# Optimization experiments

Measured on AMD Instinct MI355X. Metric: run time of the kernel, lower is better.

Reference implementation:

```python
import jax, jax.numpy as jnp
import numpy as np

B, L, Q = 2, 512, 512
E, W, D, H_NLM = 1024, 1024, 8, 32
NH = 16
HD = E // NH
SA, SO = 512, 1024
V = 8192
T = 6  # max_thought_step
SYN_H = 2048


def setup_inputs() -> dict:
    key = jax.random.key(0)
    ks = jax.random.split(key, 24)
    n = lambda k, shp, s=0.02: jax.random.normal(k, shp, dtype=jnp.float32) * s
    return {
        "x": jax.random.randint(ks[0], (B, L), 0, V),
        "num_output_q": Q,
        "emb": n(ks[1], (V, E)),
        "w_kv": n(ks[2], (E, E)),
        "w_q_sync": n(ks[3], (SA, E)),
        "wq": n(ks[4], (E, E)),
        "wk": n(ks[5], (E, E)),
        "wv": n(ks[6], (E, E)),
        "wo": n(ks[7], (E, E)),
        "ws1": n(ks[8], (E + W, SYN_H)),
        "bs1": jnp.zeros((SYN_H,), jnp.float32),
        "ws2": n(ks[9], (SYN_H, W)),
        "bs2": jnp.zeros((W,), jnp.float32),
        "nlm_w1": n(ks[10], (W, D, H_NLM), 0.1),
        "nlm_b1": jnp.zeros((W, H_NLM), jnp.float32),
        "nlm_w2": n(ks[11], (W, H_NLM), 0.1),
        "nlm_b2": jnp.zeros((W,), jnp.float32),
        "out_w": n(ks[12], (SO, V)),
        "out_b": jnp.zeros((V,), jnp.float32),
        "z_init": jax.random.normal(ks[13], (W,), dtype=jnp.float32),
        "pah_init": jax.random.normal(ks[14], (W, D), dtype=jnp.float32),
        "decay_a": jnp.zeros((SA,), jnp.float32),
        "decay_o": jnp.zeros((SO,), jnp.float32),
        "idx_la": jax.random.randint(ks[15], (SA,), 0, W),
        "idx_ra": jax.random.randint(ks[16], (SA,), 0, W),
        "idx_lo": jax.random.randint(ks[17], (SO,), 0, W),
        "idx_ro": jax.random.randint(ks[18], (SO,), 0, W),
    }


def _rope(xh, pos):
    # xh: [B, NH, S, HD]; rotate-half RoPE
    half = HD // 2
    inv = 1.0 / (10000.0 ** (jnp.arange(half, dtype=jnp.float32) / half))
    ang = pos.astype(jnp.float32)[:, None] * inv[None, :]  # [S, half]
    cos, sin = jnp.cos(ang), jnp.sin(ang)
    x1, x2 = xh[..., :half], xh[..., half:]
    return jnp.concatenate([x1 * cos - x2 * sin, x2 * cos + x1 * sin], axis=-1)


def _attention(q_in, kv, wq, wk, wv, wo):
    # causal cross-attention with RoPE on q and k
    Bq, Sq, _ = q_in.shape
    Sk = kv.shape[1]
    heads = lambda t: t.reshape(t.shape[0], t.shape[1], NH, HD).transpose(0, 2, 1, 3)
    qh = _rope(heads(q_in @ wq), jnp.arange(Sq))
    kh = _rope(heads(kv @ wk), jnp.arange(Sk))
    vh = heads(kv @ wv)
    scores = jnp.einsum('bhqd,bhkd->bhqk', qh, kh) / jnp.sqrt(jnp.float32(HD))
    i = jnp.arange(Sq)[:, None]
    j = jnp.arange(Sk)[None, :]
    scores = jnp.where(j <= i + (Sk - Sq), scores, jnp.float32(-1e30))
    out = jnp.einsum('bhqk,bhkd->bhqd', jax.nn.softmax(scores, axis=-1), vh)
    return out.transpose(0, 2, 1, 3).reshape(Bq, Sq, E) @ wo


def _compute_sync(hist, idx_l, idx_r, decay):
    # hist: list of [B,Q,W]; exponentially-decayed gather-multiply-reduce over time
    seq = jnp.stack(hist, axis=1)  # [B, Tn, Q, W]
    Tn = seq.shape[1]
    t_back = jnp.arange(Tn - 1, -1, -1, dtype=jnp.float32).reshape(1, Tn, 1, 1)
    ed = jnp.exp(-t_back * decay.reshape(1, 1, 1, -1))  # [1,Tn,1,S]
    sm = seq[..., idx_l] * ed * seq[..., idx_r]  # [B,Tn,Q,S]
    return sm.sum(axis=1) / jnp.sqrt(ed.sum(axis=1))  # [B,Q,S]


def reference(x, num_output_q, emb, w_kv, w_q_sync, wq, wk, wv, wo, ws1, bs1, ws2, bs2,
              nlm_w1, nlm_b1, nlm_w2, nlm_b2, out_w, out_b, z_init, pah_init,
              decay_a, decay_o, idx_la, idx_ra, idx_lo, idx_ro):
    emb_input = emb[x]                      # [B,L,E]
    kv = emb_input @ w_kv                   # [B,L,E]
    pah = jnp.broadcast_to(pah_init, (B, Q, W, D))
    z = jnp.broadcast_to(z_init, (B, Q, W))
    hist = [z]
    sync_a = _compute_sync(hist, idx_la, idx_ra, decay_a)
    outs = []
    for _ in range(T):
        q = sync_a @ w_q_sync               # [B,Q,E]
        attn_out = _attention(q, kv, wq, wk, wv, wo)
        pre = jnp.concatenate([attn_out, z], axis=-1)        # [B,Q,E+W]
        pre = jax.nn.gelu(pre @ ws1 + bs1) @ ws2 + bs2        # synapse -> [B,Q,W]
        pah = jnp.concatenate([pah[..., 1:], pre[..., None]], axis=-1)
        h = jax.nn.gelu(jnp.einsum('bqwd,wdh->bqwh', pah, nlm_w1) + nlm_b1)
        z = jnp.einsum('bqwh,wh->bqw', h, nlm_w2) + nlm_b2    # neuron-level model
        hist.append(z)
        sync_a = _compute_sync(hist, idx_la, idx_ra, decay_a)
        sync_o = _compute_sync(hist, idx_lo, idx_ro, decay_o)
        outs.append(sync_o @ out_w + out_b)                   # [B,Q,V]
    return jnp.stack(outs, axis=0)          # [T,B,Q,V]
```

## Files before the change

### kernel.cpp

```cpp
#include <hip/hip_runtime.h>

#define B_ 2
#define L_ 512
#define Q_ 512
#define E_ 1024
#define W_ 1024
#define D_ 8
#define H_ 32
#define NH_ 16
#define HD_ 64
#define SA_ 512
#define SO_ 1024
#define V_ 8192
#define T_ 6
#define SYNH_ 2048

#define BQ_ 1024
#define BL_ 1024

typedef __attribute__((ext_vector_type(8))) short bf16x8;
typedef __attribute__((ext_vector_type(4))) float f32x4;

__device__ __forceinline__ float gelu_f(float x) {
    const float c = 0.7978845608028654f;
    float x3 = x * x * x;
    return 0.5f * x * (1.0f + tanhf(c * (x + 0.044715f * x3)));
}

__device__ __forceinline__ unsigned short f2bf(float x) {
    unsigned int u = __float_as_uint(x);
    u += 0x7fffu + ((u >> 16) & 1u);
    return (unsigned short)(u >> 16);
}
__device__ __forceinline__ float bf2f(unsigned short h) {
    return __uint_as_float(((unsigned int)h) << 16);
}

__device__ __forceinline__ void gload16(const void* g, void* l) {
    __builtin_amdgcn_global_load_lds(
        (const __attribute__((address_space(1))) void*)g,
        (__attribute__((address_space(3))) void*)l, 16, 0, 0);
}

__global__ __launch_bounds__(256) void gemm_split_deep(
    const unsigned short* __restrict__ Ah, const unsigned short* __restrict__ Al,
    const unsigned short* __restrict__ Bh, const unsigned short* __restrict__ Bl,
    float* __restrict__ C, unsigned short* __restrict__ CHp, unsigned short* __restrict__ CLp,
    int ldc, const float* __restrict__ bias,
    int M, int N, int K, int act)
{
    constexpr int TS = 64 * 32;
    __shared__ unsigned short sAh[3][TS], sAl[3][TS], sBh[3][TS], sBl[3][TS];

    const int tid  = threadIdx.x;
    const int wave = tid >> 6;
    const int lane = tid & 63;
    const int r15 = lane & 15;
    const int r4  = lane >> 4;
    const int bm = blockIdx.y * 64;
    const int bn = blockIdx.x * 64;
    const int wm = (wave >> 1) * 32;
    const int wn = (wave & 1) * 32;

    f32x4 acc[2][2] = {};

    const int row = tid >> 2, c = tid & 3;
    const int cs = c ^ ((row >> 1) & 3);
    const size_t goffA = (size_t)(bm + row) * K + cs * 8;
    const size_t goffB = (size_t)(bn + row) * K + cs * 8;
    const int ldst = wave * 512;

    const int nk = K / 32;
    auto issue = [&](int t, int bi) {
        const size_t ka = (size_t)t * 32;
        gload16(Ah + goffA + ka, &sAh[bi][ldst]);
        gload16(Al + goffA + ka, &sAl[bi][ldst]);
        gload16(Bh + goffB + ka, &sBh[bi][ldst]);
        gload16(Bl + goffB + ka, &sBl[bi][ldst]);
    };
    issue(0, 0);
    if (nk > 1) issue(1, 1);

    for (int t = 0; t < nk; ++t) {
        if (t + 1 < nk) asm volatile("s_waitcnt vmcnt(4)" ::: "memory");
        else            asm volatile("s_waitcnt vmcnt(0)" ::: "memory");
        __syncthreads();
        if (t + 2 < nk) issue(t + 2, (t + 2) % 3);

        const int bi = t % 3;
        bf16x8 afh[2], afl[2], bfh[2], bfl[2];
#pragma unroll
        for (int i = 0; i < 2; ++i) {
            const int rr = wm + i * 16 + r15;
            const int off = rr * 32 + (r4 ^ ((rr >> 1) & 3)) * 8;
            afh[i] = *(const bf16x8*)(&sAh[bi][off]);
            afl[i] = *(const bf16x8*)(&sAl[bi][off]);
        }
#pragma unroll
        for (int j = 0; j < 2; ++j) {
            const int rr = wn + j * 16 + r15;
            const int off = rr * 32 + (r4 ^ ((rr >> 1) & 3)) * 8;
            bfh[j] = *(const bf16x8*)(&sBh[bi][off]);
            bfl[j] = *(const bf16x8*)(&sBl[bi][off]);
        }
#pragma unroll
        for (int i = 0; i < 2; ++i)
#pragma unroll
            for (int j = 0; j < 2; ++j) {
                acc[i][j] = __builtin_amdgcn_mfma_f32_16x16x32_bf16(afh[i], bfh[j], acc[i][j], 0, 0, 0);
                acc[i][j] = __builtin_amdgcn_mfma_f32_16x16x32_bf16(afh[i], bfl[j], acc[i][j], 0, 0, 0);
                acc[i][j] = __builtin_amdgcn_mfma_f32_16x16x32_bf16(afl[i], bfh[j], acc[i][j], 0, 0, 0);
            }
    }

    const int crow0 = bm + wm + r4 * 4;
    const int ccol0 = bn + wn + r15;
#pragma unroll
    for (int i = 0; i < 2; ++i) {
#pragma unroll
        for (int j = 0; j < 2; ++j) {
            const int col = ccol0 + j * 16;
            const float bv = bias ? bias[col] : 0.0f;
#pragma unroll
            for (int r = 0; r < 4; ++r) {
                const int rw = crow0 + i * 16 + r;
                float v = acc[i][j][r] + bv;
                if (act) v = gelu_f(v);
                const size_t o = (size_t)rw * ldc + col;
                if (C) C[o] = v;
                if (CHp) {
                    unsigned short hh = f2bf(v);
                    CHp[o] = hh;
                    CLp[o] = f2bf(v - bf2f(hh));
                }
            }
        }
    }
}

template<int EPI>
__global__ __launch_bounds__(256) void gemm_split_128(
    const unsigned short* __restrict__ Ah, const unsigned short* __restrict__ Al,
    const unsigned short* __restrict__ Bh, const unsigned short* __restrict__ Bl,
    float* __restrict__ C, unsigned short* __restrict__ CHp, unsigned short* __restrict__ CLp,
    int ldc, const float* __restrict__ bias,
    int M, int N, int K, int act)
{
    constexpr int TS = 128 * 32;
    __shared__ unsigned short sAh[2][TS], sAl[2][TS], sBh[2][TS], sBl[2][TS];

    const int tid  = threadIdx.x;
    const int wave = tid >> 6;
    const int lane = tid & 63;
    const int r15 = lane & 15;
    const int r4  = lane >> 4;
    const int bm = blockIdx.y * 128;
    const int bn = blockIdx.x * 128;
    const int wm = (wave >> 1) * 64;
    const int wn = (wave & 1) * 64;

    f32x4 acc[4][4] = {};

    size_t goffA[2], goffB[2];
    int ldst[2];
#pragma unroll
    for (int p2 = 0; p2 < 2; ++p2) {
        int ch = p2 * 256 + tid;
        int row = ch >> 2, c = ch & 3;
        int cs = c ^ ((row >> 1) & 3);
        goffA[p2] = (size_t)(bm + row) * K + cs * 8;
        goffB[p2] = (size_t)(bn + row) * K + cs * 8;
        ldst[p2] = (p2 * 256 + wave * 64) * 8;
    }

    const int nk = K / 32;
#pragma unroll
    for (int p2 = 0; p2 < 2; ++p2) {
        gload16(Ah + goffA[p2], &sAh[0][ldst[p2]]);
        gload16(Al + goffA[p2], &sAl[0][ldst[p2]]);
        gload16(Bh + goffB[p2], &sBh[0][ldst[p2]]);
        gload16(Bl + goffB[p2], &sBl[0][ldst[p2]]);
    }
    asm volatile("s_waitcnt vmcnt(0)" ::: "memory");
    __syncthreads();

    for (int t = 0; t < nk; ++t) {
        const int cur = t & 1;
        if (t + 1 < nk) {
            const size_t kadd = (size_t)(t + 1) * 32;
#pragma unroll
            for (int p2 = 0; p2 < 2; ++p2) {
                gload16(Ah + goffA[p2] + kadd, &sAh[cur ^ 1][ldst[p2]]);
                gload16(Al + goffA[p2] + kadd, &sAl[cur ^ 1][ldst[p2]]);
                gload16(Bh + goffB[p2] + kadd, &sBh[cur ^ 1][ldst[p2]]);
                gload16(Bl + goffB[p2] + kadd, &sBl[cur ^ 1][ldst[p2]]);
            }
        }
        bf16x8 afh[4], afl[4], bfh[4], bfl[4];
#pragma unroll
        for (int i = 0; i < 4; ++i) {
            const int rr = wm + i * 16 + r15;
            const int off = rr * 32 + (r4 ^ ((rr >> 1) & 3)) * 8;
            afh[i] = *(const bf16x8*)(&sAh[cur][off]);
            afl[i] = *(const bf16x8*)(&sAl[cur][off]);
        }
#pragma unroll
        for (int j = 0; j < 4; ++j) {
            const int rr = wn + j * 16 + r15;
            const int off = rr * 32 + (r4 ^ ((rr >> 1) & 3)) * 8;
            bfh[j] = *(const bf16x8*)(&sBh[cur][off]);
            bfl[j] = *(const bf16x8*)(&sBl[cur][off]);
        }
#pragma unroll
        for (int i = 0; i < 4; ++i)
#pragma unroll
            for (int j = 0; j < 4; ++j) {
                acc[i][j] = __builtin_amdgcn_mfma_f32_16x16x32_bf16(afh[i], bfh[j], acc[i][j], 0, 0, 0);
                acc[i][j] = __builtin_amdgcn_mfma_f32_16x16x32_bf16(afh[i], bfl[j], acc[i][j], 0, 0, 0);
                acc[i][j] = __builtin_amdgcn_mfma_f32_16x16x32_bf16(afl[i], bfh[j], acc[i][j], 0, 0, 0);
            }
        asm volatile("s_waitcnt vmcnt(0)" ::: "memory");
        __syncthreads();
    }

    if constexpr (EPI == 0) {
        const int crow0 = bm + wm + r4 * 4;
        const int ccol0 = bn + wn + r15;
#pragma unroll
        for (int i = 0; i < 4; ++i) {
#pragma unroll
            for (int j = 0; j < 4; ++j) {
                const int col = ccol0 + j * 16;
                const float bv = bias ? bias[col] : 0.0f;
#pragma unroll
                for (int r = 0; r < 4; ++r) {
                    const int rw = crow0 + i * 16 + r;
                    float v = acc[i][j][r] + bv;
                    if (act) v = gelu_f(v);
                    const size_t o = (size_t)rw * ldc + col;
                    if (C) C[o] = v;
                    if (CHp) {
                        unsigned short hh = f2bf(v);
                        CHp[o] = hh;
                        CLp[o] = f2bf(v - bf2f(hh));
                    }
                }
            }
        }
    } else {
        const int crow0 = bm + wm + r4 * 4;
#pragma unroll
        for (int i = 0; i < 4; ++i) {
#pragma unroll
            for (int r = 0; r < 4; ++r) {
                const int rw = crow0 + i * 16 + r;
                const int b = rw >> 9, q = rw & 511;
#pragma unroll
                for (int j = 0; j < 2; ++j) {
                    const int col = bn + wn + j * 16 + r15;
                    const int hh = col >> 6;
                    const int d2 = col & 31;
                    float x1 = acc[i][j][r], x2 = acc[i][j + 2][r];
                    float invf = powf(10000.0f, -(float)d2 / 32.0f);
                    float ang = (float)q * invf;
                    float cc = cosf(ang), sn = sinf(ang);
                    float o1 = x1 * cc - x2 * sn;
                    float o2 = x2 * cc + x1 * sn;
                    size_t dbase = (((size_t)b * NH_ + hh) * Q_ + q) * HD_;
                    unsigned short u1 = f2bf(o1), u2 = f2bf(o2);
                    CHp[dbase + d2] = u1;
                    CLp[dbase + d2] = f2bf(o1 - bf2f(u1));
                    CHp[dbase + d2 + 32] = u2;
                    CLp[dbase + d2 + 32] = f2bf(o2 - bf2f(u2));
                }
            }
        }
    }
}

__global__ __launch_bounds__(256) void attn_mfma(
    const unsigned short* __restrict__ qh_h, const unsigned short* __restrict__ qh_l,
    const unsigned short* __restrict__ kh_h, const unsigned short* __restrict__ kh_l,
    const unsigned short* __restrict__ vt_h, const unsigned short* __restrict__ vt_l,
    unsigned short* __restrict__ ctxH, unsigned short* __restrict__ ctxL)
{
    __shared__ unsigned short sPh[64 * 64], sPl[64 * 64];

    const int tid  = threadIdx.x;
    const int wave = tid >> 6;
    const int lane = tid & 63;
    const int r15 = lane & 15;
    const int r4  = lane >> 4;
    const int qt = blockIdx.x;
    const int h  = blockIdx.y;
    const int b  = blockIdx.z;
    const int bh = b * NH_ + h;
    const int qbase = qt * 64 + wave * 16;

    bf16x8 qa[2][2];
    {
        const unsigned short* qr_h = qh_h + ((size_t)bh * Q_ + qbase + r15) * HD_ + r4 * 8;
        const unsigned short* qr_l = qh_l + ((size_t)bh * Q_ + qbase + r15) * HD_ + r4 * 8;
        qa[0][0] = *(const bf16x8*)(qr_h);
        qa[1][0] = *(const bf16x8*)(qr_h + 32);
        qa[0][1] = *(const bf16x8*)(qr_l);
        qa[1][1] = *(const bf16x8*)(qr_l + 32);
    }

    f32x4 of[4] = {};
    float mrow[4] = {-1e30f, -1e30f, -1e30f, -1e30f};
    float lrow[4] = {};

    const unsigned short* kb_h = kh_h + (size_t)bh * L_ * HD_;
    const unsigned short* kb_l = kh_l + (size_t)bh * L_ * HD_;
    const unsigned short* vb_h = vt_h + (size_t)bh * HD_ * L_;
    const unsigned short* vb_l = vt_l + (size_t)bh * HD_ * L_;

    for (int kt = 0; kt <= qt; ++kt) {
        f32x4 sf[4] = {};
#pragma unroll
        for (int ks = 0; ks < 2; ++ks) {
#pragma unroll
            for (int j = 0; j < 4; ++j) {
                const size_t ko = (size_t)(kt * 64 + j * 16 + r15) * HD_ + ks * 32 + r4 * 8;
                bf16x8 kfh = *(const bf16x8*)(kb_h + ko);
                bf16x8 kfl = *(const bf16x8*)(kb_l + ko);
                sf[j] = __builtin_amdgcn_mfma_f32_16x16x32_bf16(qa[ks][0], kfh, sf[j], 0, 0, 0);
                sf[j] = __builtin_amdgcn_mfma_f32_16x16x32_bf16(qa[ks][0], kfl, sf[j], 0, 0, 0);
                sf[j] = __builtin_amdgcn_mfma_f32_16x16x32_bf16(qa[ks][1], kfh, sf[j], 0, 0, 0);
            }
        }

        const bool diag = (kt == qt);
#pragma unroll
        for (int j = 0; j < 4; ++j)
#pragma unroll
            for (int r = 0; r < 4; ++r) {
                float s = sf[j][r] * 0.125f;
                if (diag) {
                    int kg = kt * 64 + j * 16 + r15;
                    int qg = qt * 64 + wave * 16 + r4 * 4 + r;
                    if (kg > qg) s = -1e30f;
                }
                sf[j][r] = s;
            }

        float pv[4][4];
#pragma unroll
        for (int r = 0; r < 4; ++r) {
            float mx = fmaxf(fmaxf(sf[0][r], sf[1][r]), fmaxf(sf[2][r], sf[3][r]));
#pragma unroll
            for (int d = 1; d < 16; d <<= 1) mx = fmaxf(mx, __shfl_xor(mx, d, 64));
            float mnew = fmaxf(mrow[r], mx);
            float corr = expf(mrow[r] - mnew);
            float rs = 0.0f;
#pragma unroll
            for (int j = 0; j < 4; ++j) {
                float pp = expf(sf[j][r] - mnew);
                pv[j][r] = pp;
                rs += pp;
            }
#pragma unroll
            for (int d = 1; d < 16; d <<= 1) rs += __shfl_xor(rs, d, 64);
            lrow[r] = lrow[r] * corr + rs;
            mrow[r] = mnew;
#pragma unroll
            for (int j = 0; j < 4; ++j) of[j][r] *= corr;
        }

#pragma unroll
        for (int j = 0; j < 4; ++j)
#pragma unroll
            for (int r = 0; r < 4; ++r) {
                const int prow = wave * 16 + r4 * 4 + r;
                const int pcol = j * 16 + r15;
                const int off = prow * 64 + (pcol ^ ((prow & 7) << 3));
                unsigned short ph = f2bf(pv[j][r]);
                sPh[off] = ph;
                sPl[off] = f2bf(pv[j][r] - bf2f(ph));
            }
        __syncthreads();

#pragma unroll
        for (int ks = 0; ks < 2; ++ks) {
            const int arow = wave * 16 + r15;
            const int aoff = arow * 64 + (((ks * 32 + r4 * 8)) ^ ((arow & 7) << 3));
            bf16x8 pah = *(const bf16x8*)(sPh + aoff);
            bf16x8 pal = *(const bf16x8*)(sPl + aoff);
#pragma unroll
            for (int j = 0; j < 4; ++j) {
                const size_t vo = (size_t)(j * 16 + r15) * L_ + kt * 64 + ks * 32 + r4 * 8;
                bf16x8 vfh = *(const bf16x8*)(vb_h + vo);
                bf16x8 vfl = *(const bf16x8*)(vb_l + vo);
                of[j] = __builtin_amdgcn_mfma_f32_16x16x32_bf16(pah, vfh, of[j], 0, 0, 0);
                of[j] = __builtin_amdgcn_mfma_f32_16x16x32_bf16(pah, vfl, of[j], 0, 0, 0);
                of[j] = __builtin_amdgcn_mfma_f32_16x16x32_bf16(pal, vfh, of[j], 0, 0, 0);
            }
        }
        __syncthreads();
    }

    float linv[4];
#pragma unroll
    for (int r = 0; r < 4; ++r) linv[r] = 1.0f / lrow[r];
#pragma unroll
    for (int j = 0; j < 4; ++j)
#pragma unroll
        for (int r = 0; r < 4; ++r) {
            const int qg = qt * 64 + wave * 16 + r4 * 4 + r;
            const int dc = h * HD_ + j * 16 + r15;
            const size_t o = ((size_t)b * Q_ + qg) * E_ + dc;
            float v = of[j][r] * linv[r];
            unsigned short hh = f2bf(v);
            ctxH[o] = hh;
            ctxL[o] = f2bf(v - bf2f(hh));
        }
}

__global__ void cvt_split(const float* __restrict__ X,
                          unsigned short* __restrict__ H, unsigned short* __restrict__ L,
                          size_t n4)
{
    size_t i = (size_t)blockIdx.x * 256 + threadIdx.x;
    if (i >= n4) return;
    float4 v = ((const float4*)X)[i];
    ushort4 h, l;
    h.x = f2bf(v.x); l.x = f2bf(v.x - bf2f(h.x));
    h.y = f2bf(v.y); l.y = f2bf(v.y - bf2f(h.y));
    h.z = f2bf(v.z); l.z = f2bf(v.z - bf2f(h.z));
    h.w = f2bf(v.w); l.w = f2bf(v.w - bf2f(h.w));
    ((ushort4*)H)[i] = h;
    ((ushort4*)L)[i] = l;
}

__global__ __launch_bounds__(256) void cvt_split_T(
    const float* __restrict__ X, int R, int Cc,
    unsigned short* __restrict__ H, unsigned short* __restrict__ L)
{
    __shared__ float tile[32][33];
    const int rb = blockIdx.y * 32, cb = blockIdx.x * 32;
    const int tx = threadIdx.x & 31, ty = threadIdx.x >> 5;
#pragma unroll
    for (int r = 0; r < 32; r += 8)
        tile[ty + r][tx] = X[(size_t)(rb + ty + r) * Cc + cb + tx];
    __syncthreads();
#pragma unroll
    for (int r = 0; r < 32; r += 8) {
        float v = tile[tx][ty + r];
        unsigned short h = f2bf(v);
        unsigned short l = f2bf(v - bf2f(h));
        size_t o = (size_t)(cb + ty + r) * R + rb + tx;
        H[o] = h;
        L[o] = l;
    }
}

__global__ __launch_bounds__(256) void vtrans_split(
    const float* __restrict__ v_lin,
    unsigned short* __restrict__ H, unsigned short* __restrict__ L)
{
    __shared__ float tile[32][33];
    const int bh = blockIdx.z;
    const int b = bh >> 4, h = bh & 15;
    const int rb = blockIdx.y * 32;
    const int cb = blockIdx.x * 32;
    const int tx = threadIdx.x & 31, ty = threadIdx.x >> 5;
#pragma unroll
    for (int r = 0; r < 32; r += 8)
        tile[ty + r][tx] = v_lin[((size_t)b * L_ + rb + ty + r) * E_ + h * HD_ + cb + tx];
    __syncthreads();
#pragma unroll
    for (int r = 0; r < 32; r += 8) {
        float v = tile[tx][ty + r];
        unsigned short hh = f2bf(v);
        unsigned short ll = f2bf(v - bf2f(hh));
        size_t o = (size_t)bh * HD_ * L_ + (size_t)(cb + ty + r) * L_ + rb + tx;
        H[o] = hh;
        L[o] = ll;
    }
}

__global__ void gather_emb_split(const int* __restrict__ x, const float* __restrict__ emb,
                                 unsigned short* __restrict__ H, unsigned short* __restrict__ L) {
    size_t i = (size_t)blockIdx.x * 256 + threadIdx.x;
    const int e4n = E_ / 4;
    size_t row = i / e4n;
    int e4 = (int)(i % e4n);
    float4 v = *(((const float4*)(emb + (size_t)x[row] * E_)) + e4);
    ushort4 h, l;
    h.x = f2bf(v.x); l.x = f2bf(v.x - bf2f(h.x));
    h.y = f2bf(v.y); l.y = f2bf(v.y - bf2f(h.y));
    h.z = f2bf(v.z); l.z = f2bf(v.z - bf2f(h.z));
    h.w = f2bf(v.w); l.w = f2bf(v.w - bf2f(h.w));
    ((ushort4*)H)[i] = h;
    ((ushort4*)L)[i] = l;
}

__global__ void rope_heads_split(const float* __restrict__ lin,
                                 unsigned short* __restrict__ OH, unsigned short* __restrict__ OL,
                                 int S, int applyRope) {
    const int half = HD_ / 2;
    size_t idx = (size_t)blockIdx.x * 256 + threadIdx.x;
    size_t total = (size_t)B_ * S * NH_ * half;
    if (idx >= total) return;
    int d2 = (int)(idx % half);
    int h = (int)((idx / half) % NH_);
    int s = (int)((idx / ((size_t)half * NH_)) % S);
    int b = (int)(idx / ((size_t)half * NH_ * S));
    const float* src = lin + ((size_t)b * S + s) * E_ + h * HD_;
    float x1 = src[d2], x2 = src[d2 + half];
    float o1, o2;
    if (applyRope) {
        float invf = powf(10000.0f, -(float)d2 / (float)half);
        float ang = (float)s * invf;
        float c = cosf(ang), sn = sinf(ang);
        o1 = x1 * c - x2 * sn;
        o2 = x2 * c + x1 * sn;
    } else {
        o1 = x1; o2 = x2;
    }
    size_t dbase = (((size_t)b * NH_ + h) * S + s) * HD_;
    unsigned short h1s = f2bf(o1);
    unsigned short h2s = f2bf(o2);
    OH[dbase + d2] = h1s;
    OL[dbase + d2] = f2bf(o1 - bf2f(h1s));
    OH[dbase + d2 + half] = h2s;
    OL[dbase + d2 + half] = f2bf(o2 - bf2f(h2s));
}

__global__ void init_hist0(const float* __restrict__ z_init, float* __restrict__ hist0) {
    size_t i = (size_t)blockIdx.x * 256 + threadIdx.x;
    if (i >= (size_t)W_ * BQ_) return;
    hist0[i] = z_init[i / BQ_];
}

__global__ void init_pah(const float* __restrict__ pah_init, float* __restrict__ pah) {
    size_t i = (size_t)blockIdx.x * 256 + threadIdx.x;
    if (i >= (size_t)W_ * BQ_ * D_) return;
    int d = (int)(i % D_);
    int w = (int)(i / ((size_t)BQ_ * D_));
    pah[i] = pah_init[(size_t)w * D_ + d];
}

__global__ __launch_bounds__(256) void sync_kernel(
    const float* __restrict__ hist, int Tn,
    const int* __restrict__ idx_l, const int* __restrict__ idx_r,
    const float* __restrict__ decay,
    unsigned short* __restrict__ outH, unsigned short* __restrict__ outL, int S) {
    const int s = blockIdx.y;
    const int bq = blockIdx.x * 256 + threadIdx.x;
    const int wl = idx_l[s], wr = idx_r[s];
    const float dc = decay[s];
    float num = 0.0f, den = 0.0f;
    for (int t = 0; t < Tn; ++t) {
        float wgt = expf(-(float)(Tn - 1 - t) * dc);
        const float* hp = hist + (size_t)t * W_ * BQ_;
        num = fmaf(wgt * hp[(size_t)wl * BQ_ + bq], hp[(size_t)wr * BQ_ + bq], num);
        den += wgt;
    }
    float v = num * rsqrtf(den);
    unsigned short hh = f2bf(v);
    outH[(size_t)bq * S + s] = hh;
    outL[(size_t)bq * S + s] = f2bf(v - bf2f(hh));
}

__global__ __launch_bounds__(256) void sync_fused(
    const float* __restrict__ hist, int Tn,
    const int* __restrict__ idx_la, const int* __restrict__ idx_ra,
    const float* __restrict__ decay_a,
    unsigned short* __restrict__ saH, unsigned short* __restrict__ saL,
    const int* __restrict__ idx_lo, const int* __restrict__ idx_ro,
    const float* __restrict__ decay_o,
    unsigned short* __restrict__ soH, unsigned short* __restrict__ soL,
    int doA)
{
    const int s0 = blockIdx.y;
    const bool isA = doA && (s0 < SA_);
    const int s = isA ? s0 : (s0 - (doA ? SA_ : 0));
    const int S = isA ? SA_ : SO_;
    const int wl = isA ? idx_la[s] : idx_lo[s];
    const int wr = isA ? idx_ra[s] : idx_ro[s];
    const float dc = isA ? decay_a[s] : decay_o[s];
    unsigned short* oh = isA ? saH : soH;
    unsigned short* ol = isA ? saL : soL;
    const int bq = blockIdx.x * 256 + threadIdx.x;
    float num = 0.0f, den = 0.0f;
    for (int t = 0; t < Tn; ++t) {
        float wgt = expf(-(float)(Tn - 1 - t) * dc);
        const float* hp = hist + (size_t)t * W_ * BQ_;
        num = fmaf(wgt * hp[(size_t)wl * BQ_ + bq], hp[(size_t)wr * BQ_ + bq], num);
        den += wgt;
    }
    float v = num * rsqrtf(den);
    unsigned short hh = f2bf(v);
    oh[(size_t)bq * S + s] = hh;
    ol[(size_t)bq * S + s] = f2bf(v - bf2f(hh));
}

__global__ void copy_z_cat_split(const float* __restrict__ z,
                                 unsigned short* __restrict__ catH,
                                 unsigned short* __restrict__ catL) {
    size_t i = (size_t)blockIdx.x * 256 + threadIdx.x;
    if (i >= (size_t)BQ_ * W_) return;
    size_t bq = i / W_;
    int w = (int)(i % W_);
    float v = z[(size_t)w * BQ_ + bq];
    unsigned short hh = f2bf(v);
    size_t o = bq * (E_ + W_) + E_ + w;
    catH[o] = hh;
    catL[o] = f2bf(v - bf2f(hh));
}

__global__ __launch_bounds__(256) void nlm_kernel(
    float* __restrict__ pah,
    const float* __restrict__ pre,
    const float* __restrict__ w1,
    const float* __restrict__ b1,
    const float* __restrict__ w2,
    const float* __restrict__ b2,
    float* __restrict__ zout)
{
    const int w = blockIdx.y;
    const int bq = blockIdx.x * 256 + threadIdx.x;
    const int tid = threadIdx.x;

    __shared__ float w1s[D_ * H_];
    __shared__ float b1s[H_];
    __shared__ float w2s[H_];
    w1s[tid] = w1[(size_t)w * D_ * H_ + tid];
    if (tid < H_) {
        b1s[tid] = b1[(size_t)w * H_ + tid];
        w2s[tid] = w2[(size_t)w * H_ + tid];
    }
    __syncthreads();

    float* pp = pah + ((size_t)w * BQ_ + bq) * D_;
    float4 lo = *(float4*)pp;
    float4 hi = *(float4*)(pp + 4);
    float p[D_];
    p[0] = lo.y; p[1] = lo.z; p[2] = lo.w;
    p[3] = hi.x; p[4] = hi.y; p[5] = hi.z; p[6] = hi.w;
    p[7] = pre[(size_t)bq * W_ + w];
    *(float4*)pp = make_float4(p[0], p[1], p[2], p[3]);
    *(float4*)(pp + 4) = make_float4(p[4], p[5], p[6], p[7]);

    float zacc = b2[w];
#pragma unroll
    for (int j = 0; j < H_; ++j) {
        float a = b1s[j];
#pragma unroll
        for (int d = 0; d < D_; ++d) a = fmaf(p[d], w1s[d * H_ + j], a);
        zacc = fmaf(gelu_f(a), w2s[j], zacc);
    }
    zout[(size_t)w * BQ_ + bq] = zacc;
}

static inline void gemm64(const unsigned short* Ah, const unsigned short* Al,
                          const unsigned short* Bh, const unsigned short* Bl,
                          float* C, unsigned short* CH, unsigned short* CL, int ldc,
                          const float* bias, int M, int N, int K, int act, hipStream_t s) {
    dim3 g(N / 64, M / 64);
    gemm_split_deep<<<g, 256, 0, s>>>(Ah, Al, Bh, Bl, C, CH, CL, ldc, bias, M, N, K, act);
}
static inline void gemm128(const unsigned short* Ah, const unsigned short* Al,
                           const unsigned short* Bh, const unsigned short* Bl,
                           float* C, unsigned short* CH, unsigned short* CL, int ldc,
                           const float* bias, int M, int N, int K, int act, hipStream_t s) {
    dim3 g(N / 128, M / 128);
    gemm_split_128<0><<<g, 256, 0, s>>>(Ah, Al, Bh, Bl, C, CH, CL, ldc, bias, M, N, K, act);
}
static inline void gemm128_rope(const unsigned short* Ah, const unsigned short* Al,
                                const unsigned short* Bh, const unsigned short* Bl,
                                unsigned short* QH, unsigned short* QL,
                                int M, int N, int K, hipStream_t s) {
    dim3 g(N / 128, M / 128);
    gemm_split_128<1><<<g, 256, 0, s>>>(Ah, Al, Bh, Bl, nullptr, QH, QL, 0, nullptr, M, N, K, 0);
}

static inline void launch_cvt(const float* X, unsigned short* H, unsigned short* L,
                              size_t n, hipStream_t s) {
    size_t n4 = n / 4;
    cvt_split<<<(unsigned)((n4 + 255) / 256), 256, 0, s>>>(X, H, L, n4);
}

static inline void launch_cvtT(const float* X, int R, int C,
                               unsigned short* H, unsigned short* L, hipStream_t s) {
    dim3 g(C / 32, R / 32);
    cvt_split_T<<<g, 256, 0, s>>>(X, R, C, H, L);
}

extern "C" void kernel_launch(void* const* d_in, const int* in_sizes, int n_in,
                              void* d_out, int out_size, void* d_ws, size_t ws_size,
                              hipStream_t stream) {
    const int*   x        = (const int*)d_in[0];
    const float* emb      = (const float*)d_in[2];
    const float* w_kv     = (const float*)d_in[3];
    const float* w_q_sync = (const float*)d_in[4];
    const float* wq       = (const float*)d_in[5];
    const float* wk       = (const float*)d_in[6];
    const float* wv       = (const float*)d_in[7];
    const float* wo       = (const float*)d_in[8];
    const float* ws1      = (const float*)d_in[9];
    const float* bs1      = (const float*)d_in[10];
    const float* ws2      = (const float*)d_in[11];
    const float* bs2      = (const float*)d_in[12];
    const float* nlm_w1   = (const float*)d_in[13];
    const float* nlm_b1   = (const float*)d_in[14];
    const float* nlm_w2   = (const float*)d_in[15];
    const float* nlm_b2   = (const float*)d_in[16];
    const float* out_w    = (const float*)d_in[17];
    const float* out_b    = (const float*)d_in[18];
    const float* z_init   = (const float*)d_in[19];
    const float* pah_init = (const float*)d_in[20];
    const float* decay_a  = (const float*)d_in[21];
    const float* decay_o  = (const float*)d_in[22];
    const int*   idx_la   = (const int*)d_in[23];
    const int*   idx_ra   = (const int*)d_in[24];
    const int*   idx_lo   = (const int*)d_in[25];
    const int*   idx_ro   = (const int*)d_in[26];

    float* out = (float*)d_out;

    const size_t BQ  = BQ_;
    const size_t BL  = BL_;
    const size_t BQW = BQ * W_;
    const size_t M1  = (size_t)1024 * 1024;

    float* p = (float*)d_ws;
    auto alloc = [&](size_t n) { float* r = p; p += n; return r; };
    auto alloc_us = [&](size_t n) { unsigned short* r = (unsigned short*)p; p += n / 2; return r; };

    float* k_lin  = alloc(M1);
    float* v_lin  = alloc(M1);
    float* pre    = alloc(M1);
    float* hist   = alloc((size_t)(T_ + 1) * BQW);
    float* pah    = alloc(BQW * D_);
    float* combined = alloc((size_t)SA_ * E_);

    unsigned short* embS_h = alloc_us(M1);            unsigned short* embS_l = alloc_us(M1);
    unsigned short* wkvT_h = alloc_us(M1);            unsigned short* wkvT_l = alloc_us(M1);
    unsigned short* kvS_h  = alloc_us(M1);            unsigned short* kvS_l  = alloc_us(M1);
    unsigned short* wkT_h  = alloc_us(M1);            unsigned short* wkT_l  = alloc_us(M1);
    unsigned short* wvT_h  = alloc_us(M1);            unsigned short* wvT_l  = alloc_us(M1);
    unsigned short* wqsS_h = alloc_us(M1 / 2);        unsigned short* wqsS_l = alloc_us(M1 / 2);
    unsigned short* wqT_h  = alloc_us(M1);            unsigned short* wqT_l  = alloc_us(M1);
    unsigned short* combT_h = alloc_us(M1 / 2);       unsigned short* combT_l = alloc_us(M1 / 2);
    unsigned short* woT_h  = alloc_us(M1);            unsigned short* woT_l  = alloc_us(M1);
    unsigned short* ws1T_h = alloc_us(4 * M1);        unsigned short* ws1T_l = alloc_us(4 * M1);
    unsigned short* ws2T_h = alloc_us(2 * M1);        unsigned short* ws2T_l = alloc_us(2 * M1);
    unsigned short* outwT_h = alloc_us(8 * M1);       unsigned short* outwT_l = alloc_us(8 * M1);
    unsigned short* saS_h  = alloc_us(M1 / 2);        unsigned short* saS_l  = alloc_us(M1 / 2);
    unsigned short* ctxS_h = alloc_us(M1);            unsigned short* ctxS_l = alloc_us(M1);
    unsigned short* catS_h = alloc_us(2 * M1);        unsigned short* catS_l = alloc_us(2 * M1);
    unsigned short* h1S_h  = alloc_us(2 * M1);        unsigned short* h1S_l  = alloc_us(2 * M1);
    unsigned short* soS_h  = alloc_us(M1);            unsigned short* soS_l  = alloc_us(M1);
    unsigned short* qhS_h  = alloc_us(M1);            unsigned short* qhS_l  = alloc_us(M1);
    unsigned short* khS_h  = alloc_us(M1);            unsigned short* khS_l  = alloc_us(M1);
    unsigned short* vtS_h  = alloc_us(M1);            unsigned short* vtS_l  = alloc_us(M1);

    {
        size_t n = BL * (E_ / 4);
        gather_emb_split<<<(unsigned)((n + 255) / 256), 256, 0, stream>>>(x, emb, embS_h, embS_l);
    }
    launch_cvtT(w_kv, E_, E_, wkvT_h, wkvT_l, stream);
    gemm64(embS_h, embS_l, wkvT_h, wkvT_l, nullptr, kvS_h, kvS_l, E_, nullptr, (int)BL, E_, E_, 0, stream);
    launch_cvtT(wk, E_, E_, wkT_h, wkT_l, stream);
    launch_cvtT(wv, E_, E_, wvT_h, wvT_l, stream);
    gemm64(kvS_h, kvS_l, wkT_h, wkT_l, k_lin, nullptr, nullptr, E_, nullptr, (int)BL, E_, E_, 0, stream);
    gemm64(kvS_h, kvS_l, wvT_h, wvT_l, v_lin, nullptr, nullptr, E_, nullptr, (int)BL, E_, E_, 0, stream);
    {
        size_t n = (size_t)B_ * L_ * NH_ * (HD_ / 2);
        rope_heads_split<<<(unsigned)((n + 255) / 256), 256, 0, stream>>>(k_lin, khS_h, khS_l, L_, 1);
    }
    {
        dim3 g(HD_ / 32, L_ / 32, B_ * NH_);
        vtrans_split<<<g, 256, 0, stream>>>(v_lin, vtS_h, vtS_l);
    }
    launch_cvt(w_q_sync, wqsS_h, wqsS_l, (size_t)SA_ * E_, stream);
    launch_cvtT(wq, E_, E_, wqT_h, wqT_l, stream);
    gemm64(wqsS_h, wqsS_l, wqT_h, wqT_l, combined, nullptr, nullptr, E_, nullptr, SA_, E_, E_, 0, stream);
    launch_cvtT(combined, SA_, E_, combT_h, combT_l, stream);
    launch_cvtT(wo, E_, E_, woT_h, woT_l, stream);
    launch_cvtT(ws1, E_ + W_, SYNH_, ws1T_h, ws1T_l, stream);
    launch_cvtT(ws2, SYNH_, W_, ws2T_h, ws2T_l, stream);
    launch_cvtT(out_w, SO_, V_, outwT_h, outwT_l, stream);

    init_hist0<<<(unsigned)((BQW + 255) / 256), 256, 0, stream>>>(z_init, hist);
    init_pah<<<(unsigned)((BQW * D_ + 255) / 256), 256, 0, stream>>>(pah_init, pah);
    {
        dim3 g(BQ_ / 256, SA_);
        sync_kernel<<<g, 256, 0, stream>>>(hist, 1, idx_la, idx_ra, decay_a, saS_h, saS_l, SA_);
    }

    for (int t = 0; t < T_; ++t) {
        const float* z = hist + (size_t)t * BQW;

        gemm128_rope(saS_h, saS_l, combT_h, combT_l, qhS_h, qhS_l, (int)BQ, E_, SA_, stream);
        {
            dim3 g(Q_ / 64, NH_, B_);
            attn_mfma<<<g, 256, 0, stream>>>(qhS_h, qhS_l, khS_h, khS_l, vtS_h, vtS_l, ctxS_h, ctxS_l);
        }
        gemm64(ctxS_h, ctxS_l, woT_h, woT_l, nullptr, catS_h, catS_l, E_ + W_, nullptr, (int)BQ, E_, E_, 0, stream);
        copy_z_cat_split<<<(unsigned)((BQW + 255) / 256), 256, 0, stream>>>(z, catS_h, catS_l);

        gemm64(catS_h, catS_l, ws1T_h, ws1T_l, nullptr, h1S_h, h1S_l, SYNH_, bs1, (int)BQ, SYNH_, E_ + W_, 1, stream);
        gemm64(h1S_h, h1S_l, ws2T_h, ws2T_l, pre, nullptr, nullptr, W_, bs2, (int)BQ, W_, SYNH_, 0, stream);

        float* znext = hist + (size_t)(t + 1) * BQW;
        {
            dim3 g(BQ_ / 256, W_);
            nlm_kernel<<<g, 256, 0, stream>>>(pah, pre, nlm_w1, nlm_b1, nlm_w2, nlm_b2, znext);
        }

        int Tn = t + 2;
        int doA = (t < T_ - 1) ? 1 : 0;
        {
            dim3 g(BQ_ / 256, doA ? (SA_ + SO_) : SO_);
            sync_fused<<<g, 256, 0, stream>>>(hist, Tn, idx_la, idx_ra, decay_a, saS_h, saS_l,
                                              idx_lo, idx_ro, decay_o, soS_h, soS_l, doA);
        }

        float* out_t = out + (size_t)t * BQ * V_;
        gemm128(soS_h, soS_l, outwT_h, outwT_l, out_t, nullptr, nullptr, V_, out_b, (int)BQ, V_, SO_, 0, stream);
    }
}
```

Before: 2.551 ms.

## Stage attention K/V tiles in LDS and use raw barriers in GEMM loop

The attention kernel now copies each 64-key K and V tile (hi and lo bf16 parts) into swizzled shared memory with direct global-to-LDS loads. All four waves then read their MFMA operands from LDS instead of each wave reloading the same tile from global memory. The GEMM main loop swaps __syncthreads for a bare s_barrier plus compiler fences and tracks ring-buffer indices incrementally instead of using modulo. The attention staging is not double-buffered: it waits on vmcnt(0) and a barrier every tile, which exposes load latency and raises LDS use per block.

```diff
diff --git a/kernel.cpp b/kernel.cpp
--- a/kernel.cpp
+++ b/kernel.cpp
@@ -81,27 +81,28 @@
     issue(0, 0);
     if (nk > 1) issue(1, 1);
 
+    int bcur = 0, bnext = 2;
     for (int t = 0; t < nk; ++t) {
         if (t + 1 < nk) asm volatile("s_waitcnt vmcnt(4)" ::: "memory");
         else            asm volatile("s_waitcnt vmcnt(0)" ::: "memory");
-        __syncthreads();
-        if (t + 2 < nk) issue(t + 2, (t + 2) % 3);
-
-        const int bi = t % 3;
+        __builtin_amdgcn_s_barrier();
+        asm volatile("" ::: "memory");
+        if (t + 2 < nk) issue(t + 2, bnext);
+
         bf16x8 afh[2], afl[2], bfh[2], bfl[2];
 #pragma unroll
         for (int i = 0; i < 2; ++i) {
             const int rr = wm + i * 16 + r15;
             const int off = rr * 32 + (r4 ^ ((rr >> 1) & 3)) * 8;
-            afh[i] = *(const bf16x8*)(&sAh[bi][off]);
-            afl[i] = *(const bf16x8*)(&sAl[bi][off]);
+            afh[i] = *(const bf16x8*)(&sAh[bcur][off]);
+            afl[i] = *(const bf16x8*)(&sAl[bcur][off]);
         }
 #pragma unroll
         for (int j = 0; j < 2; ++j) {
             const int rr = wn + j * 16 + r15;
             const int off = rr * 32 + (r4 ^ ((rr >> 1) & 3)) * 8;
-            bfh[j] = *(const bf16x8*)(&sBh[bi][off]);
-            bfl[j] = *(const bf16x8*)(&sBl[bi][off]);
+            bfh[j] = *(const bf16x8*)(&sBh[bcur][off]);
+            bfl[j] = *(const bf16x8*)(&sBl[bcur][off]);
         }
 #pragma unroll
         for (int i = 0; i < 2; ++i)
@@ -111,6 +112,9 @@
                 acc[i][j] = __builtin_amdgcn_mfma_f32_16x16x32_bf16(afh[i], bfl[j], acc[i][j], 0, 0, 0);
                 acc[i][j] = __builtin_amdgcn_mfma_f32_16x16x32_bf16(afl[i], bfh[j], acc[i][j], 0, 0, 0);
             }
+        asm volatile("" ::: "memory");
+        bcur = (bcur == 2) ? 0 : bcur + 1;
+        bnext = (bnext == 2) ? 0 : bnext + 1;
     }
 
     const int crow0 = bm + wm + r4 * 4;
@@ -284,6 +288,8 @@
     const unsigned short* __restrict__ vt_h, const unsigned short* __restrict__ vt_l,
     unsigned short* __restrict__ ctxH, unsigned short* __restrict__ ctxL)
 {
+    __shared__ unsigned short sKh[64 * 64], sKl[64 * 64];
+    __shared__ unsigned short sVh[64 * 64], sVl[64 * 64];
     __shared__ unsigned short sPh[64 * 64], sPl[64 * 64];
 
     const int tid  = threadIdx.x;
@@ -311,20 +317,41 @@
     float mrow[4] = {-1e30f, -1e30f, -1e30f, -1e30f};
     float lrow[4] = {};
 
+    const int row0 = tid >> 3,        i70 = tid & 7;
+    const int row1 = 32 + (tid >> 3), i71 = tid & 7;
+    const int ko0 = row0 * 64 + ((i70 * 8) ^ ((row0 & 7) << 3));
+    const int ko1 = row1 * 64 + ((i71 * 8) ^ ((row1 & 7) << 3));
+    const size_t vo0 = (size_t)row0 * L_ + ((i70 * 8) ^ ((row0 & 7) << 3));
+    const size_t vo1 = (size_t)row1 * L_ + ((i71 * 8) ^ ((row1 & 7) << 3));
+    const int ld0 = wave * 512;
+    const int ld1 = 2048 + wave * 512;
+
     const unsigned short* kb_h = kh_h + (size_t)bh * L_ * HD_;
     const unsigned short* kb_l = kh_l + (size_t)bh * L_ * HD_;
     const unsigned short* vb_h = vt_h + (size_t)bh * HD_ * L_;
     const unsigned short* vb_l = vt_l + (size_t)bh * HD_ * L_;
 
     for (int kt = 0; kt <= qt; ++kt) {
+        gload16(kb_h + kt * 4096 + ko0, sKh + ld0);
+        gload16(kb_h + kt * 4096 + ko1, sKh + ld1);
+        gload16(kb_l + kt * 4096 + ko0, sKl + ld0);
+        gload16(kb_l + kt * 4096 + ko1, sKl + ld1);
+        gload16(vb_h + vo0 + kt * 64, sVh + ld0);
+        gload16(vb_h + vo1 + kt * 64, sVh + ld1);
+        gload16(vb_l + vo0 + kt * 64, sVl + ld0);
+        gload16(vb_l + vo1 + kt * 64, sVl + ld1);
+        asm volatile("s_waitcnt vmcnt(0)" ::: "memory");
+        __syncthreads();
+
         f32x4 sf[4] = {};
 #pragma unroll
         for (int ks = 0; ks < 2; ++ks) {
 #pragma unroll
             for (int j = 0; j < 4; ++j) {
-                const size_t ko = (size_t)(kt * 64 + j * 16 + r15) * HD_ + ks * 32 + r4 * 8;
-                bf16x8 kfh = *(const bf16x8*)(kb_h + ko);
-                bf16x8 kfl = *(const bf16x8*)(kb_l + ko);
+                const int kr = j * 16 + r15;
+                const int off = kr * 64 + (((ks * 32 + r4 * 8)) ^ ((kr & 7) << 3));
+                bf16x8 kfh = *(const bf16x8*)(sKh + off);
+                bf16x8 kfl = *(const bf16x8*)(sKl + off);
                 sf[j] = __builtin_amdgcn_mfma_f32_16x16x32_bf16(qa[ks][0], kfh, sf[j], 0, 0, 0);
                 sf[j] = __builtin_amdgcn_mfma_f32_16x16x32_bf16(qa[ks][0], kfl, sf[j], 0, 0, 0);
                 sf[j] = __builtin_amdgcn_mfma_f32_16x16x32_bf16(qa[ks][1], kfh, sf[j], 0, 0, 0);
@@ -389,9 +416,10 @@
             bf16x8 pal = *(const bf16x8*)(sPl + aoff);
 #pragma unroll
             for (int j = 0; j < 4; ++j) {
-                const size_t vo = (size_t)(j * 16 + r15) * L_ + kt * 64 + ks * 32 + r4 * 8;
-                bf16x8 vfh = *(const bf16x8*)(vb_h + vo);
-                bf16x8 vfl = *(const bf16x8*)(vb_l + vo);
+                const int vrow = j * 16 + r15;
+                const int voff = vrow * 64 + (((ks * 32 + r4 * 8)) ^ ((vrow & 7) << 3));
+                bf16x8 vfh = *(const bf16x8*)(sVh + voff);
+                bf16x8 vfl = *(const bf16x8*)(sVl + voff);
                 of[j] = __builtin_amdgcn_mfma_f32_16x16x32_bf16(pah, vfh, of[j], 0, 0, 0);
                 of[j] = __builtin_amdgcn_mfma_f32_16x16x32_bf16(pah, vfl, of[j], 0, 0, 0);
                 of[j] = __builtin_amdgcn_mfma_f32_16x16x32_bf16(pal, vfh, of[j], 0, 0, 0);
```

After: 2.401 ms. -5.9%, faster.
